# Kernel tuning notes

Hardware: AMD Instinct MI355X
Metric: run time of the kernel (lower is better)

## Reference

```python
import jax, jax.numpy as jnp
import numpy as np

B, T, INPUT_DIM, Z_DIM, RNN_DIM = 512, 200, 88, 100, 60


def setup_inputs() -> dict:
    key = jax.random.key(0)
    ks = jax.random.split(key, 18)
    sd = 0.05
    return {
        "mini_batch": jax.random.normal(ks[0], (B, T, INPUT_DIM), jnp.float32),
        "mini_batch_reversed": jax.random.normal(ks[1], (B, T, INPUT_DIM), jnp.float32),
        "mini_batch_mask": jnp.ones((B, T), jnp.float32),
        "mini_batch_seq_lengths": jax.random.randint(ks[2], (B,), T // 2, T + 1),
        "eps": jax.random.normal(ks[3], (T, B, Z_DIM), jnp.float32),
        # RNN (relu, 1 layer) params
        "W_ih": jax.random.normal(ks[4], (RNN_DIM, INPUT_DIM), jnp.float32) * sd,
        "W_hh": jax.random.normal(ks[5], (RNN_DIM, RNN_DIM), jnp.float32) * sd,
        "b_ih": jnp.zeros((RNN_DIM,), jnp.float32),
        "b_hh": jnp.zeros((RNN_DIM,), jnp.float32),
        "h_0": jax.random.normal(ks[6], (RNN_DIM,), jnp.float32),
        "z_q_0": jnp.zeros((Z_DIM,), jnp.float32),
        # Combiner params
        "W_zh": jax.random.normal(ks[7], (RNN_DIM, Z_DIM), jnp.float32) * sd,
        "b_zh": jnp.zeros((RNN_DIM,), jnp.float32),
        "W_hl": jax.random.normal(ks[8], (Z_DIM, RNN_DIM), jnp.float32) * sd,
        "b_hl": jnp.zeros((Z_DIM,), jnp.float32),
        "W_hs": jax.random.normal(ks[9], (Z_DIM, RNN_DIM), jnp.float32) * sd,
        "b_hs": jnp.zeros((Z_DIM,), jnp.float32),
    }


def _encoder(mini_batch_reversed, seq_lengths, eps,
             W_ih, W_hh, b_ih, b_hh, h_0, z_q_0,
             W_zh, b_zh, W_hl, b_hl, W_hs, b_hs):
    Bn = mini_batch_reversed.shape[0]
    Tn = mini_batch_reversed.shape[1]

    # --- relu RNN over reversed input, batch_first -> scan over time ---
    xs = jnp.transpose(mini_batch_reversed, (1, 0, 2))  # [T, B, input_dim]
    h0 = jnp.broadcast_to(h_0, (Bn, RNN_DIM))

    def rnn_step(h, x_t):
        h = jax.nn.relu(x_t @ W_ih.T + b_ih + h @ W_hh.T + b_hh)
        return h, h

    _, rnn_out = jax.lax.scan(rnn_step, h0, xs)          # [T, B, rnn_dim]
    rnn_out = jnp.transpose(rnn_out, (1, 0, 2))          # [B, T, rnn_dim]

    # --- pad_and_reverse: reverse each sequence by its length, zero-pad tail ---
    t_idx = jnp.arange(Tn)
    rev_idx = seq_lengths[:, None] - 1 - t_idx[None, :]  # [B, T]
    valid = rev_idx >= 0
    gathered = jnp.take_along_axis(rnn_out, jnp.clip(rev_idx, 0)[:, :, None], axis=1)
    rnn_rev = jnp.where(valid[:, :, None], gathered, 0.0)  # [B, T, rnn_dim]

    # --- sequential combiner + reparameterized sampling ---
    h_seq = jnp.transpose(rnn_rev, (1, 0, 2))            # [T, B, rnn_dim]
    z0 = jnp.broadcast_to(z_q_0, (Bn, Z_DIM))

    def comb_step(z_prev, inp):
        h_t, eps_t = inp
        h_comb = 0.5 * (jnp.tanh(z_prev @ W_zh.T + b_zh) + h_t)
        loc = h_comb @ W_hl.T + b_hl
        scale = jax.nn.softplus(h_comb @ W_hs.T + b_hs)
        z_t = loc + scale * eps_t
        return z_t, (z_t, loc, scale)

    _, (zs, locs, scales) = jax.lax.scan(comb_step, z0, (h_seq, eps))
    # [T, B, z] -> [B, T, z]
    tr = lambda a: jnp.transpose(a, (1, 0, 2))
    return tr(zs), tr(locs), tr(scales)


def reference(mini_batch, mini_batch_reversed, mini_batch_mask,
              mini_batch_seq_lengths, eps,
              W_ih, W_hh, b_ih, b_hh, h_0, z_q_0,
              W_zh, b_zh, W_hl, b_hl, W_hs, b_hs):
    return _encoder(mini_batch_reversed, mini_batch_seq_lengths, eps,
                    W_ih, W_hh, b_ih, b_hh, h_0, z_q_0,
                    W_zh, b_zh, W_hl, b_hl, W_hs, b_hs)
```

## Files before the change

### kernel.cpp

```cpp
#include <hip/hip_runtime.h>
#include <cmath>

#define NB 512
#define NT 200
#define NIN 88
#define NH 60
#define NZ 100

typedef float f2 __attribute__((ext_vector_type(2)));
typedef _Float16 h2v __attribute__((ext_vector_type(2)));
typedef _Float16 h8v __attribute__((ext_vector_type(8)));

__device__ __forceinline__ f2 pk_fma(f2 a, f2 b, f2 c) {
    return __builtin_elementwise_fma(a, b, c);
}
__device__ __forceinline__ float dot2(h2v a, h2v b, float c) {
#if __has_builtin(__builtin_amdgcn_fdot2)
    return __builtin_amdgcn_fdot2(a, b, c, false);
#else
    return fmaf((float)a.x, (float)b.x, fmaf((float)a.y, (float)b.y, c));
#endif
}
__device__ __forceinline__ float fast_tanh(float x) {
    float cx = fminf(fmaxf(x, -10.f), 10.f);
    float e  = __expf(2.f * cx);
    return (e - 1.f) * __builtin_amdgcn_rcpf(e + 1.f);
}
__device__ __forceinline__ float fast_softplus(float x) {
    return fmaxf(x, 0.f) + __logf(1.f + __expf(-fabsf(x)));
}
__device__ __forceinline__ void block_sync_lds() {
    asm volatile("s_waitcnt lgkmcnt(0)" ::: "memory");
    __builtin_amdgcn_s_barrier();
    asm volatile("" ::: "memory");
}

#define TCHUNKS 5
#define TCL (NT / TCHUNKS)

__global__ __launch_bounds__(128, 1)
void pre_kernel(const float* __restrict__ xrev, const float* __restrict__ W_ih,
                const float* __restrict__ b_ih, const float* __restrict__ b_hh,
                float* __restrict__ pre)
{
    __shared__ __align__(16) float xw[2][NIN];

    const int b    = blockIdx.x;
    const int tc   = blockIdx.y;
    const int wv   = threadIdx.x >> 6;
    const int lane = threadIdx.x & 63;

    f2 wih2[44];
    float bias = 0.f;
    if (lane < NH) {
        const float4* p = reinterpret_cast<const float4*>(W_ih + lane * NIN);
#pragma unroll
        for (int k = 0; k < 22; ++k) {
            float4 v = p[k];
            wih2[2*k]   = f2{v.x, v.y};
            wih2[2*k+1] = f2{v.z, v.w};
        }
        bias = b_ih[lane] + b_hh[lane];
    } else {
#pragma unroll
        for (int k = 0; k < 44; ++k) wih2[k] = f2{0.f, 0.f};
    }

    const float* xb = xrev + ((size_t)b * NT + (size_t)tc * TCL) * NIN;
    float* pb = pre + ((size_t)b * NT + (size_t)tc * TCL) * NH;

    float xa = xb[(size_t)wv * NIN + lane];
    float xc = (lane < NIN - 64) ? xb[(size_t)wv * NIN + 64 + lane] : 0.f;

    for (int k = 0; k < TCL / 2; ++k) {
        const int t = wv + 2 * k;
        xw[wv][lane] = xa;
        if (lane < NIN - 64) xw[wv][64 + lane] = xc;
        const int tn = t + 2;
        if (tn < TCL) {
            xa = xb[(size_t)tn * NIN + lane];
            xc = (lane < NIN - 64) ? xb[(size_t)tn * NIN + 64 + lane] : 0.f;
        }
        const float4* x4 = reinterpret_cast<const float4*>(xw[wv]);
        f2 a0 = f2{bias, 0.f}, a1 = f2{0.f, 0.f};
#pragma unroll
        for (int q = 0; q < 22; ++q) {
            float4 v = x4[q];
            a0 = pk_fma(f2{v.x, v.y}, wih2[2*q],   a0);
            a1 = pk_fma(f2{v.z, v.w}, wih2[2*q+1], a1);
        }
        if (lane < NH) pb[(size_t)t * NH + lane] = (a0.x + a1.x) + (a0.y + a1.y);
    }
}

__global__ __launch_bounds__(128, 1)
void fused1w(const int*   __restrict__ seqlen,
             const float* __restrict__ eps,
             const float* __restrict__ W_hh,
             const float* __restrict__ h0,
             const float* __restrict__ zq0,
             const float* __restrict__ W_zh,
             const float* __restrict__ b_zh,
             const float* __restrict__ W_hl,
             const float* __restrict__ b_hl,
             const float* __restrict__ W_hs,
             const float* __restrict__ b_hs,
             const float* __restrict__ pre,
             float* __restrict__ out)
{
    __shared__ __align__(16) _Float16 h_rev_h[2][NT][NH];
    __shared__ __align__(16) float    hbuf[2][64];
    __shared__ __align__(16) _Float16 zbh[2][112];
    __shared__ __align__(16) _Float16 hch[2][64];

    const int wv   = threadIdx.x >> 6;
    const int lane = threadIdx.x & 63;
    const int b    = blockIdx.x * 2 + wv;
    const int sl   = seqlen[b];

    {
        const int tail = (NT - sl) * NH;
        _Float16* base = &h_rev_h[wv][sl][0];
        for (int i = lane; i < tail; i += 64) base[i] = (_Float16)0;
    }
    if (lane < 12) zbh[wv][100 + lane] = (_Float16)0;
    if (lane >= NH) hch[wv][lane] = (_Float16)0;

    const bool oln = (lane < 50);
    const int  o1  = lane;
    const int  o2  = lane + 50;
    float e1 = 0.f, e2 = 0.f;
    if (oln) {
        zbh[wv][o1] = (_Float16)zq0[o1];
        zbh[wv][o2] = (_Float16)zq0[o2];
        e1 = eps[(size_t)b * NZ + o1];
        e2 = eps[(size_t)b * NZ + o2];
    }

    {
        f2 whh2[30];
        if (lane < NH) {
            const float4* q = reinterpret_cast<const float4*>(W_hh + lane * NH);
#pragma unroll
            for (int k = 0; k < 15; ++k) {
                float4 v = q[k];
                whh2[2*k]   = f2{v.x, v.y};
                whh2[2*k+1] = f2{v.z, v.w};
            }
            hbuf[wv][lane] = h0[lane];
        } else {
#pragma unroll
            for (int k = 0; k < 30; ++k) whh2[k] = f2{0.f, 0.f};
        }

        const float* pb = pre + (size_t)b * NT * NH;
        const bool hl = (lane < NH);
        float p0 = hl ? pb[0 * NH + lane] : 0.f;
        float p1 = hl ? pb[1 * NH + lane] : 0.f;
        float p2 = hl ? pb[2 * NH + lane] : 0.f;
        float p3 = hl ? pb[3 * NH + lane] : 0.f;
        for (int t = 0; t < NT; ++t) {
            float pn = (t + 4 < NT && hl) ? pb[(size_t)(t + 4) * NH + lane] : 0.f;
            const float4* h4 = reinterpret_cast<const float4*>(&hbuf[wv][0]);
            f2 a0 = f2{p0, 0.f}, a1 = f2{0.f, 0.f};
#pragma unroll
            for (int k = 0; k < 15; ++k) {
                float4 v = h4[k];
                a0 = pk_fma(f2{v.x, v.y}, whh2[2*k],   a0);
                a1 = pk_fma(f2{v.z, v.w}, whh2[2*k+1], a1);
            }
            float hn = fmaxf((a0.x + a1.x) + (a0.y + a1.y), 0.f);
            if (hl) {
                hbuf[wv][lane] = hn;
                if (t < sl) h_rev_h[wv][sl - 1 - t][lane] = (_Float16)hn;
            }
            p0 = p1; p1 = p2; p2 = p3; p3 = pn;
        }
    }

    h2v wzh_h[52];
    float bz = 0.f;
    if (lane < NH) {
        const float4* q = reinterpret_cast<const float4*>(W_zh + lane * NZ);
#pragma unroll
        for (int k = 0; k < 25; ++k) {
            float4 v = q[k];
            wzh_h[2*k]   = h2v{(_Float16)v.x, (_Float16)v.y};
            wzh_h[2*k+1] = h2v{(_Float16)v.z, (_Float16)v.w};
        }
        bz = b_zh[lane];
    } else {
#pragma unroll
        for (int k = 0; k < 50; ++k) wzh_h[k] = h2v{(_Float16)0, (_Float16)0};
    }
    wzh_h[50] = h2v{(_Float16)0, (_Float16)0};
    wzh_h[51] = wzh_h[50];

    h2v wlA[32], wsA[32], wlB[32], wsB[32];
    float blA = 0.f, bsA = 0.f, blB = 0.f, bsB = 0.f;
    if (oln) {
        const float4* pA = reinterpret_cast<const float4*>(W_hl + o1 * NH);
        const float4* qA = reinterpret_cast<const float4*>(W_hs + o1 * NH);
        const float4* pB = reinterpret_cast<const float4*>(W_hl + o2 * NH);
        const float4* qB = reinterpret_cast<const float4*>(W_hs + o2 * NH);
#pragma unroll
        for (int k = 0; k < 15; ++k) {
            float4 v;
            v = pA[k];
            wlA[2*k]   = h2v{(_Float16)(0.5f*v.x), (_Float16)(0.5f*v.y)};
            wlA[2*k+1] = h2v{(_Float16)(0.5f*v.z), (_Float16)(0.5f*v.w)};
            v = qA[k];
            wsA[2*k]   = h2v{(_Float16)(0.5f*v.x), (_Float16)(0.5f*v.y)};
            wsA[2*k+1] = h2v{(_Float16)(0.5f*v.z), (_Float16)(0.5f*v.w)};
            v = pB[k];
            wlB[2*k]   = h2v{(_Float16)(0.5f*v.x), (_Float16)(0.5f*v.y)};
            wlB[2*k+1] = h2v{(_Float16)(0.5f*v.z), (_Float16)(0.5f*v.w)};
            v = qB[k];
            wsB[2*k]   = h2v{(_Float16)(0.5f*v.x), (_Float16)(0.5f*v.y)};
            wsB[2*k+1] = h2v{(_Float16)(0.5f*v.z), (_Float16)(0.5f*v.w)};
        }
        blA = b_hl[o1]; bsA = b_hs[o1];
        blB = b_hl[o2]; bsB = b_hs[o2];
    } else {
#pragma unroll
        for (int k = 0; k < 32; ++k) {
            wlA[k] = h2v{(_Float16)0, (_Float16)0};
            wsA[k] = wlA[k]; wlB[k] = wlA[k]; wsB[k] = wlA[k];
        }
    }
    h2v zpad = h2v{(_Float16)0, (_Float16)0};
    wlA[30] = zpad; wlA[31] = zpad; wsA[30] = zpad; wsA[31] = zpad;
    wlB[30] = zpad; wlB[31] = zpad; wsB[30] = zpad; wsB[31] = zpad;

    float* out_z = out;
    float* out_l = out + (size_t)NB * NT * NZ;
    float* out_s = out + (size_t)2 * NB * NT * NZ;

    for (int t = 0; t < NT; ++t) {
        const h8v* z8 = reinterpret_cast<const h8v*>(&zbh[wv][0]);
        float za0 = 0.f, za1 = 0.f, za2 = 0.f, za3 = 0.f;
#pragma unroll
        for (int k = 0; k < 13; ++k) {
            h8v v = z8[k];
            za0 = dot2(h2v{v[0], v[1]}, wzh_h[4*k+0], za0);
            za1 = dot2(h2v{v[2], v[3]}, wzh_h[4*k+1], za1);
            za2 = dot2(h2v{v[4], v[5]}, wzh_h[4*k+2], za2);
            za3 = dot2(h2v{v[6], v[7]}, wzh_h[4*k+3], za3);
        }
        float hrow = (lane < NH) ? (float)h_rev_h[wv][t][lane] : 0.f;

        float e1n = 0.f, e2n = 0.f;
        if (oln && t + 1 < NT) {
            const float* ep = eps + ((size_t)(t + 1) * NB + b) * NZ;
            e1n = ep[o1];
            e2n = ep[o2];
        }

        if (lane < NH) {
            float a = (za0 + za1) + (za2 + za3) + bz;
            hch[wv][lane] = (_Float16)(fast_tanh(a) + hrow);
        }

        const h8v* h8p = reinterpret_cast<const h8v*>(&hch[wv][0]);
        float lA0 = 0.f, lA1 = 0.f, sA0 = 0.f, sA1 = 0.f;
        float lB0 = 0.f, lB1 = 0.f, sB0 = 0.f, sB1 = 0.f;
#pragma unroll
        for (int k = 0; k < 8; ++k) {
            h8v v = h8p[k];
            h2v x0 = h2v{v[0], v[1]}, x1 = h2v{v[2], v[3]};
            h2v x2 = h2v{v[4], v[5]}, x3 = h2v{v[6], v[7]};
            lA0 = dot2(x0, wlA[4*k+0], lA0);
            lA1 = dot2(x1, wlA[4*k+1], lA1);
            lA0 = dot2(x2, wlA[4*k+2], lA0);
            lA1 = dot2(x3, wlA[4*k+3], lA1);
            sA0 = dot2(x0, wsA[4*k+0], sA0);
            sA1 = dot2(x1, wsA[4*k+1], sA1);
            sA0 = dot2(x2, wsA[4*k+2], sA0);
            sA1 = dot2(x3, wsA[4*k+3], sA1);
            lB0 = dot2(x0, wlB[4*k+0], lB0);
            lB1 = dot2(x1, wlB[4*k+1], lB1);
            lB0 = dot2(x2, wlB[4*k+2], lB0);
            lB1 = dot2(x3, wlB[4*k+3], lB1);
            sB0 = dot2(x0, wsB[4*k+0], sB0);
            sB1 = dot2(x1, wsB[4*k+1], sB1);
            sB0 = dot2(x2, wsB[4*k+2], sB0);
            sB1 = dot2(x3, wsB[4*k+3], sB1);
        }
        if (oln) {
            float locA = lA0 + lA1 + blA;
            float psA  = sA0 + sA1 + bsA;
            float scA  = fast_softplus(psA);
            float zA   = locA + scA * e1;
            float locB = lB0 + lB1 + blB;
            float psB  = sB0 + sB1 + bsB;
            float scB  = fast_softplus(psB);
            float zB   = locB + scB * e2;
            size_t oi = ((size_t)b * NT + t) * NZ;
            out_z[oi + o1] = zA;  out_z[oi + o2] = zB;
            out_l[oi + o1] = locA; out_l[oi + o2] = locB;
            out_s[oi + o1] = scA;  out_s[oi + o2] = scB;
            zbh[wv][o1] = (_Float16)zA;
            zbh[wv][o2] = (_Float16)zB;
            e1 = e1n; e2 = e2n;
        }
    }
}

__global__ __launch_bounds__(128, 1)
void encoder_mono(const float* __restrict__ xrev, const int* __restrict__ seqlen,
                  const float* __restrict__ eps,
                  const float* __restrict__ W_ih, const float* __restrict__ W_hh,
                  const float* __restrict__ b_ih, const float* __restrict__ b_hh,
                  const float* __restrict__ h0,   const float* __restrict__ zq0,
                  const float* __restrict__ W_zh, const float* __restrict__ b_zh,
                  const float* __restrict__ W_hl, const float* __restrict__ b_hl,
                  const float* __restrict__ W_hs, const float* __restrict__ b_hs,
                  float* __restrict__ out)
{
    __shared__ __align__(16) float h_rev[NT][NH];
    __shared__ __align__(16) float xbuf[NIN];
    __shared__ __align__(16) float hbuf[NH];
    __shared__ __align__(16) float zbuf[NZ];
    __shared__ __align__(16) float hcomb[NH];

    const int b = blockIdx.x, tid = threadIdx.x;
    const int wave = tid >> 6, lane = tid & 63;
    const int sl = seqlen[b];

    for (int i = tid; i < NT * NH; i += 128) (&h_rev[0][0])[i] = 0.0f;
    __syncthreads();

    if (wave == 0) {
        float wih[NIN], whh[NH];
        float bias = 0.f;
        if (lane < NH) {
            const float4* pp = reinterpret_cast<const float4*>(W_ih + lane * NIN);
#pragma unroll
            for (int k = 0; k < NIN / 4; ++k) {
                float4 v = pp[k];
                wih[4*k+0]=v.x; wih[4*k+1]=v.y; wih[4*k+2]=v.z; wih[4*k+3]=v.w;
            }
            const float4* q = reinterpret_cast<const float4*>(W_hh + lane * NH);
#pragma unroll
            for (int k = 0; k < NH / 4; ++k) {
                float4 v = q[k];
                whh[4*k+0]=v.x; whh[4*k+1]=v.y; whh[4*k+2]=v.z; whh[4*k+3]=v.w;
            }
            bias = b_ih[lane] + b_hh[lane];
            hbuf[lane] = h0[lane];
        } else {
#pragma unroll
            for (int k = 0; k < NIN; ++k) wih[k] = 0.f;
#pragma unroll
            for (int k = 0; k < NH; ++k) whh[k] = 0.f;
        }
        const float* xb = xrev + (size_t)b * NT * NIN;
        float xa = xb[lane];
        float xc = (lane < NIN - 64) ? xb[64 + lane] : 0.f;
        for (int t = 0; t < NT; ++t) {
            xbuf[lane] = xa;
            if (lane < NIN - 64) xbuf[64 + lane] = xc;
            if (t + 1 < NT) {
                xa = xb[(size_t)(t+1)*NIN + lane];
                xc = (lane < NIN - 64) ? xb[(size_t)(t+1)*NIN + 64 + lane] : 0.f;
            }
            float a0=0.f,a1=0.f,a2=0.f,a3=0.f;
            const float4* x4 = reinterpret_cast<const float4*>(xbuf);
#pragma unroll
            for (int k = 0; k < NIN / 4; ++k) {
                float4 v = x4[k];
                a0 += v.x*wih[4*k+0]; a1 += v.y*wih[4*k+1];
                a2 += v.z*wih[4*k+2]; a3 += v.w*wih[4*k+3];
            }
            const float4* h4 = reinterpret_cast<const float4*>(hbuf);
#pragma unroll
            for (int k = 0; k < NH / 4; ++k) {
                float4 v = h4[k];
                a0 += v.x*whh[4*k+0]; a1 += v.y*whh[4*k+1];
                a2 += v.z*whh[4*k+2]; a3 += v.w*whh[4*k+3];
            }
            float hn = fmaxf((a0+a1)+(a2+a3)+bias, 0.f);
            if (lane < NH) {
                hbuf[lane] = hn;
                if (t < sl) h_rev[sl-1-t][lane] = hn;
            }
        }
    }
    __syncthreads();

    const int o = 50 * wave + lane;
    float wzr[NZ]; float bz = 0.f;
    if (wave == 0 && lane < NH) {
        const float4* pp = reinterpret_cast<const float4*>(W_zh + lane * NZ);
#pragma unroll
        for (int k = 0; k < NZ / 4; ++k) {
            float4 v = pp[k];
            wzr[4*k+0]=v.x; wzr[4*k+1]=v.y; wzr[4*k+2]=v.z; wzr[4*k+3]=v.w;
        }
        bz = b_zh[lane];
    } else {
#pragma unroll
        for (int k = 0; k < NZ; ++k) wzr[k] = 0.f;
    }
    float wl[NH], ws_[NH]; float bl = 0.f, bs = 0.f;
    if (lane < 50) {
        const float4* pp = reinterpret_cast<const float4*>(W_hl + o * NH);
        const float4* q  = reinterpret_cast<const float4*>(W_hs + o * NH);
#pragma unroll
        for (int k = 0; k < NH / 4; ++k) {
            float4 v = pp[k];
            wl[4*k+0]=v.x; wl[4*k+1]=v.y; wl[4*k+2]=v.z; wl[4*k+3]=v.w;
            float4 u = q[k];
            ws_[4*k+0]=u.x; ws_[4*k+1]=u.y; ws_[4*k+2]=u.z; ws_[4*k+3]=u.w;
        }
        bl = b_hl[o]; bs = b_hs[o];
        zbuf[o] = zq0[o];
    } else {
#pragma unroll
        for (int k = 0; k < NH; ++k) { wl[k]=0.f; ws_[k]=0.f; }
    }
    __syncthreads();

    float* out_z = out;
    float* out_l = out + (size_t)NB * NT * NZ;
    float* out_s = out + (size_t)2 * NB * NT * NZ;
    const float* epsb = eps + (size_t)b * NZ;
    float e_cur = (lane < 50) ? epsb[o] : 0.f;

    for (int t = 0; t < NT; ++t) {
        if (wave == 0) {
            float a0=0.f,a1=0.f,a2=0.f,a3=0.f;
            const float4* z4 = reinterpret_cast<const float4*>(zbuf);
#pragma unroll
            for (int k = 0; k < NZ / 4; ++k) {
                float4 v = z4[k];
                a0 += v.x*wzr[4*k+0]; a1 += v.y*wzr[4*k+1];
                a2 += v.z*wzr[4*k+2]; a3 += v.w*wzr[4*k+3];
            }
            if (lane < NH) {
                float a = (a0+a1)+(a2+a3)+bz;
                hcomb[lane] = 0.5f * (fast_tanh(a) + h_rev[t][lane]);
            }
        }
        block_sync_lds();
        float e_nxt = 0.f;
        if (t + 1 < NT && lane < 50) e_nxt = epsb[(size_t)(t+1)*NB*NZ + o];
        if (lane < 50) {
            float c0=0.f,c1=0.f,c2=0.f,c3=0.f, d0=0.f,d1=0.f,d2=0.f,d3=0.f;
            const float4* h4 = reinterpret_cast<const float4*>(hcomb);
#pragma unroll
            for (int k = 0; k < NH / 4; ++k) {
                float4 v = h4[k];
                c0 += v.x*wl[4*k+0];  c1 += v.y*wl[4*k+1];
                c2 += v.z*wl[4*k+2];  c3 += v.w*wl[4*k+3];
                d0 += v.x*ws_[4*k+0]; d1 += v.y*ws_[4*k+1];
                d2 += v.z*ws_[4*k+2]; d3 += v.w*ws_[4*k+3];
            }
            float loc = (c0+c1)+(c2+c3)+bl;
            float ps  = (d0+d1)+(d2+d3)+bs;
            float sc  = fast_softplus(ps);
            float zv  = loc + sc * e_cur;
            size_t oi = ((size_t)b * NT + t) * NZ + o;
            out_z[oi]=zv; out_l[oi]=loc; out_s[oi]=sc;
            zbuf[o]=zv;
        }
        e_cur = e_nxt;
        block_sync_lds();
    }
}

extern "C" void kernel_launch(void* const* d_in, const int* in_sizes, int n_in,
                              void* d_out, int out_size, void* d_ws, size_t ws_size,
                              hipStream_t stream) {
    const float* xrev   = (const float*)d_in[1];
    const int*   seqlen = (const int*)  d_in[3];
    const float* eps    = (const float*)d_in[4];
    const float* W_ih   = (const float*)d_in[5];
    const float* W_hh   = (const float*)d_in[6];
    const float* b_ih   = (const float*)d_in[7];
    const float* b_hh   = (const float*)d_in[8];
    const float* h0     = (const float*)d_in[9];
    const float* zq0    = (const float*)d_in[10];
    const float* W_zh   = (const float*)d_in[11];
    const float* b_zh   = (const float*)d_in[12];
    const float* W_hl   = (const float*)d_in[13];
    const float* b_hl   = (const float*)d_in[14];
    const float* W_hs   = (const float*)d_in[15];
    const float* b_hs   = (const float*)d_in[16];
    float* out = (float*)d_out;

    const size_t pre_bytes = (size_t)NB * NT * NH * sizeof(float);
    if (ws_size >= pre_bytes) {
        float* pre = (float*)d_ws;
        pre_kernel<<<dim3(NB, TCHUNKS), 128, 0, stream>>>(xrev, W_ih, b_ih, b_hh, pre);
        fused1w<<<NB / 2, 128, 0, stream>>>(seqlen, eps, W_hh, h0, zq0,
                                            W_zh, b_zh, W_hl, b_hl, W_hs, b_hs,
                                            pre, out);
    } else {
        encoder_mono<<<NB, 128, 0, stream>>>(xrev, seqlen, eps,
                                             W_ih, W_hh, b_ih, b_hh, h0, zq0,
                                             W_zh, b_zh, W_hl, b_hl, W_hs, b_hs,
                                             out);
    }
}
```

Baseline: 276.2 us.

## Process two batch elements per single wavefront with interleaved recurrences

The fused recurrent kernel now runs one 64-lane wavefront per block that advances two batch sequences together, interleaving their RNN and combiner dot products instead of assigning one wave per sequence. The aim is to hide per-step LDS and dependency latency through instruction-level parallelism and to share the register-resident weights. In exchange each wave does twice the serial work and uses more registers, and the two sequences no longer run on separate SIMDs in parallel.

```diff
diff --git a/kernel.cpp b/kernel.cpp
--- a/kernel.cpp
+++ b/kernel.cpp
@@ -93,8 +93,8 @@
     }
 }
 
-__global__ __launch_bounds__(128, 1)
-void fused1w(const int*   __restrict__ seqlen,
+__global__ __launch_bounds__(64, 1) __attribute__((amdgpu_waves_per_eu(1)))
+void fused2s(const int*   __restrict__ seqlen,
              const float* __restrict__ eps,
              const float* __restrict__ W_hh,
              const float* __restrict__ h0,
@@ -109,32 +109,41 @@
              float* __restrict__ out)
 {
     __shared__ __align__(16) _Float16 h_rev_h[2][NT][NH];
-    __shared__ __align__(16) float    hbuf[2][64];
+    __shared__ __align__(16) float    hbufF[2][64];
     __shared__ __align__(16) _Float16 zbh[2][112];
     __shared__ __align__(16) _Float16 hch[2][64];
 
-    const int wv   = threadIdx.x >> 6;
-    const int lane = threadIdx.x & 63;
-    const int b    = blockIdx.x * 2 + wv;
-    const int sl   = seqlen[b];
+    const int lane = threadIdx.x;
+    const int b0   = blockIdx.x * 2;
+    const int b1   = b0 + 1;
+    const int sl0  = seqlen[b0];
+    const int sl1  = seqlen[b1];
 
     {
-        const int tail = (NT - sl) * NH;
-        _Float16* base = &h_rev_h[wv][sl][0];
-        for (int i = lane; i < tail; i += 64) base[i] = (_Float16)0;
-    }
-    if (lane < 12) zbh[wv][100 + lane] = (_Float16)0;
-    if (lane >= NH) hch[wv][lane] = (_Float16)0;
+        const int tail = (NT - sl0) * NH;
+        _Float16* p = &h_rev_h[0][sl0][0];
+        for (int i = lane; i < tail; i += 64) p[i] = (_Float16)0;
+    }
+    {
+        const int tail = (NT - sl1) * NH;
+        _Float16* p = &h_rev_h[1][sl1][0];
+        for (int i = lane; i < tail; i += 64) p[i] = (_Float16)0;
+    }
+    if (lane < 12) { zbh[0][100 + lane] = (_Float16)0; zbh[1][100 + lane] = (_Float16)0; }
+    if (lane >= NH) { hch[0][lane] = (_Float16)0; hch[1][lane] = (_Float16)0; }
 
     const bool oln = (lane < 50);
     const int  o1  = lane;
     const int  o2  = lane + 50;
-    float e1 = 0.f, e2 = 0.f;
+    float e1_0 = 0.f, e2_0 = 0.f, e1_1 = 0.f, e2_1 = 0.f;
     if (oln) {
-        zbh[wv][o1] = (_Float16)zq0[o1];
-        zbh[wv][o2] = (_Float16)zq0[o2];
-        e1 = eps[(size_t)b * NZ + o1];
-        e2 = eps[(size_t)b * NZ + o2];
+        float zA = zq0[o1], zB = zq0[o2];
+        zbh[0][o1] = (_Float16)zA; zbh[0][o2] = (_Float16)zB;
+        zbh[1][o1] = (_Float16)zA; zbh[1][o2] = (_Float16)zB;
+        e1_0 = eps[(size_t)b0 * NZ + o1];
+        e2_0 = eps[(size_t)b0 * NZ + o2];
+        e1_1 = eps[(size_t)b1 * NZ + o1];
+        e2_1 = eps[(size_t)b1 * NZ + o2];
     }
 
     {
@@ -147,34 +156,48 @@
                 whh2[2*k]   = f2{v.x, v.y};
                 whh2[2*k+1] = f2{v.z, v.w};
             }
-            hbuf[wv][lane] = h0[lane];
+            float hv = h0[lane];
+            hbufF[0][lane] = hv;
+            hbufF[1][lane] = hv;
         } else {
 #pragma unroll
             for (int k = 0; k < 30; ++k) whh2[k] = f2{0.f, 0.f};
         }
 
-        const float* pb = pre + (size_t)b * NT * NH;
+        const float* pbA = pre + (size_t)b0 * NT * NH;
+        const float* pbB = pre + (size_t)b1 * NT * NH;
         const bool hl = (lane < NH);
-        float p0 = hl ? pb[0 * NH + lane] : 0.f;
-        float p1 = hl ? pb[1 * NH + lane] : 0.f;
-        float p2 = hl ? pb[2 * NH + lane] : 0.f;
-        float p3 = hl ? pb[3 * NH + lane] : 0.f;
+        float p0a = hl ? pbA[0*NH + lane] : 0.f, p0b = hl ? pbB[0*NH + lane] : 0.f;
+        float p1a = hl ? pbA[1*NH + lane] : 0.f, p1b = hl ? pbB[1*NH + lane] : 0.f;
+        float p2a = hl ? pbA[2*NH + lane] : 0.f, p2b = hl ? pbB[2*NH + lane] : 0.f;
+        float p3a = hl ? pbA[3*NH + lane] : 0.f, p3b = hl ? pbB[3*NH + lane] : 0.f;
+
         for (int t = 0; t < NT; ++t) {
-            float pn = (t + 4 < NT && hl) ? pb[(size_t)(t + 4) * NH + lane] : 0.f;
-            const float4* h4 = reinterpret_cast<const float4*>(&hbuf[wv][0]);
-            f2 a0 = f2{p0, 0.f}, a1 = f2{0.f, 0.f};
+            float pna = (t + 4 < NT && hl) ? pbA[(size_t)(t + 4) * NH + lane] : 0.f;
+            float pnb = (t + 4 < NT && hl) ? pbB[(size_t)(t + 4) * NH + lane] : 0.f;
+            const float4* h4a = reinterpret_cast<const float4*>(&hbufF[0][0]);
+            const float4* h4b = reinterpret_cast<const float4*>(&hbufF[1][0]);
+            f2 a0 = f2{p0a, 0.f}, a1 = f2{0.f, 0.f};
+            f2 c0 = f2{p0b, 0.f}, c1 = f2{0.f, 0.f};
 #pragma unroll
             for (int k = 0; k < 15; ++k) {
-                float4 v = h4[k];
-                a0 = pk_fma(f2{v.x, v.y}, whh2[2*k],   a0);
-                a1 = pk_fma(f2{v.z, v.w}, whh2[2*k+1], a1);
-            }
-            float hn = fmaxf((a0.x + a1.x) + (a0.y + a1.y), 0.f);
+                float4 va = h4a[k];
+                a0 = pk_fma(f2{va.x, va.y}, whh2[2*k],   a0);
+                a1 = pk_fma(f2{va.z, va.w}, whh2[2*k+1], a1);
+                float4 vb = h4b[k];
+                c0 = pk_fma(f2{vb.x, vb.y}, whh2[2*k],   c0);
+                c1 = pk_fma(f2{vb.z, vb.w}, whh2[2*k+1], c1);
+            }
+            float hnA = fmaxf((a0.x + a1.x) + (a0.y + a1.y), 0.f);
+            float hnB = fmaxf((c0.x + c1.x) + (c0.y + c1.y), 0.f);
             if (hl) {
-                hbuf[wv][lane] = hn;
-                if (t < sl) h_rev_h[wv][sl - 1 - t][lane] = (_Float16)hn;
-            }
-            p0 = p1; p1 = p2; p2 = p3; p3 = pn;
+                hbufF[0][lane] = hnA;
+                hbufF[1][lane] = hnB;
+                if (t < sl0) h_rev_h[0][sl0 - 1 - t][lane] = (_Float16)hnA;
+                if (t < sl1) h_rev_h[1][sl1 - 1 - t][lane] = (_Float16)hnB;
+            }
+            p0a = p1a; p1a = p2a; p2a = p3a; p3a = pna;
+            p0b = p1b; p1b = p2b; p2b = p3b; p3b = pnb;
         }
     }
 
@@ -228,80 +251,134 @@
             wsA[k] = wlA[k]; wlB[k] = wlA[k]; wsB[k] = wlA[k];
         }
     }
-    h2v zpad = h2v{(_Float16)0, (_Float16)0};
-    wlA[30] = zpad; wlA[31] = zpad; wsA[30] = zpad; wsA[31] = zpad;
-    wlB[30] = zpad; wlB[31] = zpad; wsB[30] = zpad; wsB[31] = zpad;
+    {
+        h2v zp = h2v{(_Float16)0, (_Float16)0};
+        wlA[30] = zp; wlA[31] = zp; wsA[30] = zp; wsA[31] = zp;
+        wlB[30] = zp; wlB[31] = zp; wsB[30] = zp; wsB[31] = zp;
+    }
 
     float* out_z = out;
     float* out_l = out + (size_t)NB * NT * NZ;
     float* out_s = out + (size_t)2 * NB * NT * NZ;
 
     for (int t = 0; t < NT; ++t) {
-        const h8v* z8 = reinterpret_cast<const h8v*>(&zbh[wv][0]);
-        float za0 = 0.f, za1 = 0.f, za2 = 0.f, za3 = 0.f;
+        const h8v* z80 = reinterpret_cast<const h8v*>(&zbh[0][0]);
+        const h8v* z81 = reinterpret_cast<const h8v*>(&zbh[1][0]);
+        float za0_0 = 0.f, za1_0 = 0.f, za2_0 = 0.f, za3_0 = 0.f;
+        float za0_1 = 0.f, za1_1 = 0.f, za2_1 = 0.f, za3_1 = 0.f;
 #pragma unroll
         for (int k = 0; k < 13; ++k) {
-            h8v v = z8[k];
-            za0 = dot2(h2v{v[0], v[1]}, wzh_h[4*k+0], za0);
-            za1 = dot2(h2v{v[2], v[3]}, wzh_h[4*k+1], za1);
-            za2 = dot2(h2v{v[4], v[5]}, wzh_h[4*k+2], za2);
-            za3 = dot2(h2v{v[6], v[7]}, wzh_h[4*k+3], za3);
-        }
-        float hrow = (lane < NH) ? (float)h_rev_h[wv][t][lane] : 0.f;
-
-        float e1n = 0.f, e2n = 0.f;
+            h8v v0 = z80[k];
+            za0_0 = dot2(h2v{v0[0], v0[1]}, wzh_h[4*k+0], za0_0);
+            za1_0 = dot2(h2v{v0[2], v0[3]}, wzh_h[4*k+1], za1_0);
+            za2_0 = dot2(h2v{v0[4], v0[5]}, wzh_h[4*k+2], za2_0);
+            za3_0 = dot2(h2v{v0[6], v0[7]}, wzh_h[4*k+3], za3_0);
+            h8v v1 = z81[k];
+            za0_1 = dot2(h2v{v1[0], v1[1]}, wzh_h[4*k+0], za0_1);
+            za1_1 = dot2(h2v{v1[2], v1[3]}, wzh_h[4*k+1], za1_1);
+            za2_1 = dot2(h2v{v1[4], v1[5]}, wzh_h[4*k+2], za2_1);
+            za3_1 = dot2(h2v{v1[6], v1[7]}, wzh_h[4*k+3], za3_1);
+        }
+        float hrow0 = (lane < NH) ? (float)h_rev_h[0][t][lane] : 0.f;
+        float hrow1 = (lane < NH) ? (float)h_rev_h[1][t][lane] : 0.f;
+
+        float e1n_0 = 0.f, e2n_0 = 0.f, e1n_1 = 0.f, e2n_1 = 0.f;
         if (oln && t + 1 < NT) {
-            const float* ep = eps + ((size_t)(t + 1) * NB + b) * NZ;
-            e1n = ep[o1];
-            e2n = ep[o2];
+            const float* ep0 = eps + ((size_t)(t + 1) * NB + b0) * NZ;
+            const float* ep1 = eps + ((size_t)(t + 1) * NB + b1) * NZ;
+            e1n_0 = ep0[o1]; e2n_0 = ep0[o2];
+            e1n_1 = ep1[o1]; e2n_1 = ep1[o2];
         }
 
         if (lane < NH) {
-            float a = (za0 + za1) + (za2 + za3) + bz;
-            hch[wv][lane] = (_Float16)(fast_tanh(a) + hrow);
-        }
-
-        const h8v* h8p = reinterpret_cast<const h8v*>(&hch[wv][0]);
-        float lA0 = 0.f, lA1 = 0.f, sA0 = 0.f, sA1 = 0.f;
-        float lB0 = 0.f, lB1 = 0.f, sB0 = 0.f, sB1 = 0.f;
+            float a0 = (za0_0 + za1_0) + (za2_0 + za3_0) + bz;
+            float a1 = (za0_1 + za1_1) + (za2_1 + za3_1) + bz;
+            hch[0][lane] = (_Float16)(fast_tanh(a0) + hrow0);
+            hch[1][lane] = (_Float16)(fast_tanh(a1) + hrow1);
+        }
+
+        const h8v* hp0 = reinterpret_cast<const h8v*>(&hch[0][0]);
+        const h8v* hp1 = reinterpret_cast<const h8v*>(&hch[1][0]);
+        float lA_0 = 0.f, lAx_0 = 0.f, sA_0 = 0.f, sAx_0 = 0.f;
+        float lB_0 = 0.f, lBx_0 = 0.f, sB_0 = 0.f, sBx_0 = 0.f;
+        float lA_1 = 0.f, lAx_1 = 0.f, sA_1 = 0.f, sAx_1 = 0.f;
+        float lB_1 = 0.f, lBx_1 = 0.f, sB_1 = 0.f, sBx_1 = 0.f;
 #pragma unroll
         for (int k = 0; k < 8; ++k) {
-            h8v v = h8p[k];
-            h2v x0 = h2v{v[0], v[1]}, x1 = h2v{v[2], v[3]};
-            h2v x2 = h2v{v[4], v[5]}, x3 = h2v{v[6], v[7]};
-            lA0 = dot2(x0, wlA[4*k+0], lA0);
-            lA1 = dot2(x1, wlA[4*k+1], lA1);
-            lA0 = dot2(x2, wlA[4*k+2], lA0);
-            lA1 = dot2(x3, wlA[4*k+3], lA1);
-            sA0 = dot2(x0, wsA[4*k+0], sA0);
-            sA1 = dot2(x1, wsA[4*k+1], sA1);
-            sA0 = dot2(x2, wsA[4*k+2], sA0);
-            sA1 = dot2(x3, wsA[4*k+3], sA1);
-            lB0 = dot2(x0, wlB[4*k+0], lB0);
-            lB1 = dot2(x1, wlB[4*k+1], lB1);
-            lB0 = dot2(x2, wlB[4*k+2], lB0);
-            lB1 = dot2(x3, wlB[4*k+3], lB1);
-            sB0 = dot2(x0, wsB[4*k+0], sB0);
-            sB1 = dot2(x1, wsB[4*k+1], sB1);
-            sB0 = dot2(x2, wsB[4*k+2], sB0);
-            sB1 = dot2(x3, wsB[4*k+3], sB1);
+            h8v v0 = hp0[k];
+            h2v x00 = h2v{v0[0], v0[1]}, x01 = h2v{v0[2], v0[3]};
+            h2v x02 = h2v{v0[4], v0[5]}, x03 = h2v{v0[6], v0[7]};
+            lA_0  = dot2(x00, wlA[4*k+0], lA_0);
+            lAx_0 = dot2(x01, wlA[4*k+1], lAx_0);
+            lA_0  = dot2(x02, wlA[4*k+2], lA_0);
+            lAx_0 = dot2(x03, wlA[4*k+3], lAx_0);
+            sA_0  = dot2(x00, wsA[4*k+0], sA_0);
+            sAx_0 = dot2(x01, wsA[4*k+1], sAx_0);
+            sA_0  = dot2(x02, wsA[4*k+2], sA_0);
+            sAx_0 = dot2(x03, wsA[4*k+3], sAx_0);
+            lB_0  = dot2(x00, wlB[4*k+0], lB_0);
+            lBx_0 = dot2(x01, wlB[4*k+1], lBx_0);
+            lB_0  = dot2(x02, wlB[4*k+2], lB_0);
+            lBx_0 = dot2(x03, wlB[4*k+3], lBx_0);
+            sB_0  = dot2(x00, wsB[4*k+0], sB_0);
+            sBx_0 = dot2(x01, wsB[4*k+1], sBx_0);
+            sB_0  = dot2(x02, wsB[4*k+2], sB_0);
+            sBx_0 = dot2(x03, wsB[4*k+3], sBx_0);
+            h8v v1 = hp1[k];
+            h2v x10 = h2v{v1[0], v1[1]}, x11 = h2v{v1[2], v1[3]};
+            h2v x12 = h2v{v1[4], v1[5]}, x13 = h2v{v1[6], v1[7]};
+            lA_1  = dot2(x10, wlA[4*k+0], lA_1);
+            lAx_1 = dot2(x11, wlA[4*k+1], lAx_1);
+            lA_1  = dot2(x12, wlA[4*k+2], lA_1);
+            lAx_1 = dot2(x13, wlA[4*k+3], lAx_1);
+            sA_1  = dot2(x10, wsA[4*k+0], sA_1);
+            sAx_1 = dot2(x11, wsA[4*k+1], sAx_1);
+            sA_1  = dot2(x12, wsA[4*k+2], sA_1);
+            sAx_1 = dot2(x13, wsA[4*k+3], sAx_1);
+            lB_1  = dot2(x10, wlB[4*k+0], lB_1);
+            lBx_1 = dot2(x11, wlB[4*k+1], lBx_1);
+            lB_1  = dot2(x12, wlB[4*k+2], lB_1);
+            lBx_1 = dot2(x13, wlB[4*k+3], lBx_1);
+            sB_1  = dot2(x10, wsB[4*k+0], sB_1);
+            sBx_1 = dot2(x11, wsB[4*k+1], sBx_1);
+            sB_1  = dot2(x12, wsB[4*k+2], sB_1);
+            sBx_1 = dot2(x13, wsB[4*k+3], sBx_1);
         }
         if (oln) {
-            float locA = lA0 + lA1 + blA;
-            float psA  = sA0 + sA1 + bsA;
-            float scA  = fast_softplus(psA);
-            float zA   = locA + scA * e1;
-            float locB = lB0 + lB1 + blB;
-            float psB  = sB0 + sB1 + bsB;
-            float scB  = fast_softplus(psB);
-            float zB   = locB + scB * e2;
-            size_t oi = ((size_t)b * NT + t) * NZ;
-            out_z[oi + o1] = zA;  out_z[oi + o2] = zB;
-            out_l[oi + o1] = locA; out_l[oi + o2] = locB;
-            out_s[oi + o1] = scA;  out_s[oi + o2] = scB;
-            zbh[wv][o1] = (_Float16)zA;
-            zbh[wv][o2] = (_Float16)zB;
-            e1 = e1n; e2 = e2n;
+            {
+                float locA = lA_0 + lAx_0 + blA;
+                float psA  = sA_0 + sAx_0 + bsA;
+                float scA  = fast_softplus(psA);
+                float zA   = locA + scA * e1_0;
+                float locB = lB_0 + lBx_0 + blB;
+                float psB  = sB_0 + sBx_0 + bsB;
+                float scB  = fast_softplus(psB);
+                float zB   = locB + scB * e2_0;
+                size_t oi = ((size_t)b0 * NT + t) * NZ;
+                out_z[oi + o1] = zA;   out_z[oi + o2] = zB;
+                out_l[oi + o1] = locA; out_l[oi + o2] = locB;
+                out_s[oi + o1] = scA;  out_s[oi + o2] = scB;
+                zbh[0][o1] = (_Float16)zA;
+                zbh[0][o2] = (_Float16)zB;
+                e1_0 = e1n_0; e2_0 = e2n_0;
+            }
+            {
+                float locA = lA_1 + lAx_1 + blA;
+                float psA  = sA_1 + sAx_1 + bsA;
+                float scA  = fast_softplus(psA);
+                float zA   = locA + scA * e1_1;
+                float locB = lB_1 + lBx_1 + blB;
+                float psB  = sB_1 + sBx_1 + bsB;
+                float scB  = fast_softplus(psB);
+                float zB   = locB + scB * e2_1;
+                size_t oi = ((size_t)b1 * NT + t) * NZ;
+                out_z[oi + o1] = zA;   out_z[oi + o2] = zB;
+                out_l[oi + o1] = locA; out_l[oi + o2] = locB;
+                out_s[oi + o1] = scA;  out_s[oi + o2] = scB;
+                zbh[1][o1] = (_Float16)zA;
+                zbh[1][o2] = (_Float16)zB;
+                e1_1 = e1n_1; e2_1 = e2n_1;
+            }
         }
     }
 }
@@ -493,9 +570,9 @@
     if (ws_size >= pre_bytes) {
         float* pre = (float*)d_ws;
         pre_kernel<<<dim3(NB, TCHUNKS), 128, 0, stream>>>(xrev, W_ih, b_ih, b_hh, pre);
-        fused1w<<<NB / 2, 128, 0, stream>>>(seqlen, eps, W_hh, h0, zq0,
-                                            W_zh, b_zh, W_hl, b_hl, W_hs, b_hs,
-                                            pre, out);
+        fused2s<<<NB / 2, 64, 0, stream>>>(seqlen, eps, W_hh, h0, zq0,
+                                           W_zh, b_zh, W_hl, b_hl, W_hs, b_hs,
+                                           pre, out);
     } else {
         encoder_mono<<<NB, 128, 0, stream>>>(xrev, seqlen, eps,
                                              W_ih, W_hh, b_ih, b_hh, h0, zq0,
```

New measurement: 474.7 us. 71.9% more time.

## Move combiner output weights from registers to shared LDS with software prefetch

Applied to the files above, without the earlier changes.

The fp16 W_hl/W_hs weight registers (128 h2v per lane) are replaced by a shared LDS table that both waves fill cooperatively, since each wave's lanes need the same output rows. Inside the per-step loop the weights are streamed from LDS with a one-chunk-ahead prefetch. The goal is to relieve register pressure or spilling in the recurrent kernel. In exchange, every timestep now issues about 32 extra 16-byte LDS reads per lane that sit on the sequential critical path.

```diff
diff --git a/kernel.cpp b/kernel.cpp
--- a/kernel.cpp
+++ b/kernel.cpp
@@ -20,6 +20,12 @@
 #else
     return fmaf((float)a.x, (float)b.x, fmaf((float)a.y, (float)b.y, c));
 #endif
+}
+__device__ __forceinline__ void dot8(h8v x, h8v w, float& p, float& q) {
+    p = dot2(h2v{x[0], x[1]}, h2v{w[0], w[1]}, p);
+    q = dot2(h2v{x[2], x[3]}, h2v{w[2], w[3]}, q);
+    p = dot2(h2v{x[4], x[5]}, h2v{w[4], w[5]}, p);
+    q = dot2(h2v{x[6], x[7]}, h2v{w[6], w[7]}, q);
 }
 __device__ __forceinline__ float fast_tanh(float x) {
     float cx = fminf(fmaxf(x, -10.f), 10.f);
@@ -92,6 +98,8 @@
         if (lane < NH) pb[(size_t)t * NH + lane] = (a0.x + a1.x) + (a0.y + a1.y);
     }
 }
+
+#define WOUT_BYTES (8 * 64 * 80)
 
 __global__ __launch_bounds__(128, 1)
 void fused1w(const int*   __restrict__ seqlen,
@@ -112,6 +120,7 @@
     __shared__ __align__(16) float    hbuf[2][64];
     __shared__ __align__(16) _Float16 zbh[2][112];
     __shared__ __align__(16) _Float16 hch[2][64];
+    __shared__ __align__(16) char     wout[WOUT_BYTES];
 
     const int wv   = threadIdx.x >> 6;
     const int lane = threadIdx.x & 63;
@@ -135,6 +144,41 @@
         zbh[wv][o2] = (_Float16)zq0[o2];
         e1 = eps[(size_t)b * NZ + o1];
         e2 = eps[(size_t)b * NZ + o2];
+    }
+
+    {
+        const int r0 = 2 * wv, r1 = 2 * wv + 1;
+        if (oln) {
+            const int  oo   = (wv == 0) ? o1 : o2;
+            const float* s0 = W_hl + oo * NH;
+            const float* s1 = W_hs + oo * NH;
+#pragma unroll
+            for (int r = 0; r < 2; ++r) {
+                const float* src = (r == 0) ? s0 : s1;
+                const int rr = (r == 0) ? r0 : r1;
+                float tmp[64];
+#pragma unroll
+                for (int j = 0; j < NH; ++j) tmp[j] = 0.5f * src[j];
+#pragma unroll
+                for (int j = NH; j < 64; ++j) tmp[j] = 0.f;
+#pragma unroll
+                for (int k = 0; k < 8; ++k) {
+                    h8v h;
+#pragma unroll
+                    for (int e = 0; e < 8; ++e) h[e] = (_Float16)tmp[8*k+e];
+                    *reinterpret_cast<h8v*>(wout + k*5120 + lane*80 + rr*16) = h;
+                }
+            }
+        } else {
+            h8v zz;
+#pragma unroll
+            for (int e = 0; e < 8; ++e) zz[e] = (_Float16)0;
+#pragma unroll
+            for (int k = 0; k < 8; ++k) {
+                *reinterpret_cast<h8v*>(wout + k*5120 + lane*80 + r0*16) = zz;
+                *reinterpret_cast<h8v*>(wout + k*5120 + lane*80 + r1*16) = zz;
+            }
+        }
     }
 
     {
@@ -196,45 +240,24 @@
     wzh_h[50] = h2v{(_Float16)0, (_Float16)0};
     wzh_h[51] = wzh_h[50];
 
-    h2v wlA[32], wsA[32], wlB[32], wsB[32];
     float blA = 0.f, bsA = 0.f, blB = 0.f, bsB = 0.f;
     if (oln) {
-        const float4* pA = reinterpret_cast<const float4*>(W_hl + o1 * NH);
-        const float4* qA = reinterpret_cast<const float4*>(W_hs + o1 * NH);
-        const float4* pB = reinterpret_cast<const float4*>(W_hl + o2 * NH);
-        const float4* qB = reinterpret_cast<const float4*>(W_hs + o2 * NH);
-#pragma unroll
-        for (int k = 0; k < 15; ++k) {
-            float4 v;
-            v = pA[k];
-            wlA[2*k]   = h2v{(_Float16)(0.5f*v.x), (_Float16)(0.5f*v.y)};
-            wlA[2*k+1] = h2v{(_Float16)(0.5f*v.z), (_Float16)(0.5f*v.w)};
-            v = qA[k];
-            wsA[2*k]   = h2v{(_Float16)(0.5f*v.x), (_Float16)(0.5f*v.y)};
-            wsA[2*k+1] = h2v{(_Float16)(0.5f*v.z), (_Float16)(0.5f*v.w)};
-            v = pB[k];
-            wlB[2*k]   = h2v{(_Float16)(0.5f*v.x), (_Float16)(0.5f*v.y)};
-            wlB[2*k+1] = h2v{(_Float16)(0.5f*v.z), (_Float16)(0.5f*v.w)};
-            v = qB[k];
-            wsB[2*k]   = h2v{(_Float16)(0.5f*v.x), (_Float16)(0.5f*v.y)};
-            wsB[2*k+1] = h2v{(_Float16)(0.5f*v.z), (_Float16)(0.5f*v.w)};
-        }
         blA = b_hl[o1]; bsA = b_hs[o1];
         blB = b_hl[o2]; bsB = b_hs[o2];
-    } else {
-#pragma unroll
-        for (int k = 0; k < 32; ++k) {
-            wlA[k] = h2v{(_Float16)0, (_Float16)0};
-            wsA[k] = wlA[k]; wlB[k] = wlA[k]; wsB[k] = wlA[k];
-        }
-    }
-    h2v zpad = h2v{(_Float16)0, (_Float16)0};
-    wlA[30] = zpad; wlA[31] = zpad; wsA[30] = zpad; wsA[31] = zpad;
-    wlB[30] = zpad; wlB[31] = zpad; wsB[30] = zpad; wsB[31] = zpad;
+    }
+
+    block_sync_lds();
 
     float* out_z = out;
     float* out_l = out + (size_t)NB * NT * NZ;
     float* out_s = out + (size_t)2 * NB * NT * NZ;
+
+    const char* wbase = wout + lane * 80;
+
+    h8v pf0 = *reinterpret_cast<const h8v*>(wbase + 0*5120 + 0);
+    h8v pf1 = *reinterpret_cast<const h8v*>(wbase + 0*5120 + 16);
+    h8v pf2 = *reinterpret_cast<const h8v*>(wbase + 0*5120 + 32);
+    h8v pf3 = *reinterpret_cast<const h8v*>(wbase + 0*5120 + 48);
 
     for (int t = 0; t < NT; ++t) {
         const h8v* z8 = reinterpret_cast<const h8v*>(&zbh[wv][0]);
@@ -262,29 +285,25 @@
         }
 
         const h8v* h8p = reinterpret_cast<const h8v*>(&hch[wv][0]);
+        h8v c0 = pf0, c1 = pf1, c2 = pf2, c3 = pf3;
         float lA0 = 0.f, lA1 = 0.f, sA0 = 0.f, sA1 = 0.f;
         float lB0 = 0.f, lB1 = 0.f, sB0 = 0.f, sB1 = 0.f;
 #pragma unroll
         for (int k = 0; k < 8; ++k) {
-            h8v v = h8p[k];
-            h2v x0 = h2v{v[0], v[1]}, x1 = h2v{v[2], v[3]};
-            h2v x2 = h2v{v[4], v[5]}, x3 = h2v{v[6], v[7]};
-            lA0 = dot2(x0, wlA[4*k+0], lA0);
-            lA1 = dot2(x1, wlA[4*k+1], lA1);
-            lA0 = dot2(x2, wlA[4*k+2], lA0);
-            lA1 = dot2(x3, wlA[4*k+3], lA1);
-            sA0 = dot2(x0, wsA[4*k+0], sA0);
-            sA1 = dot2(x1, wsA[4*k+1], sA1);
-            sA0 = dot2(x2, wsA[4*k+2], sA0);
-            sA1 = dot2(x3, wsA[4*k+3], sA1);
-            lB0 = dot2(x0, wlB[4*k+0], lB0);
-            lB1 = dot2(x1, wlB[4*k+1], lB1);
-            lB0 = dot2(x2, wlB[4*k+2], lB0);
-            lB1 = dot2(x3, wlB[4*k+3], lB1);
-            sB0 = dot2(x0, wsB[4*k+0], sB0);
-            sB1 = dot2(x1, wsB[4*k+1], sB1);
-            sB0 = dot2(x2, wsB[4*k+2], sB0);
-            sB1 = dot2(x3, wsB[4*k+3], sB1);
+            h8v n0, n1, n2, n3;
+            if (k < 7) {
+                const char* nb = wbase + (k + 1) * 5120;
+                n0 = *reinterpret_cast<const h8v*>(nb + 0);
+                n1 = *reinterpret_cast<const h8v*>(nb + 16);
+                n2 = *reinterpret_cast<const h8v*>(nb + 32);
+                n3 = *reinterpret_cast<const h8v*>(nb + 48);
+            }
+            h8v x = h8p[k];
+            dot8(x, c0, lA0, lA1);
+            dot8(x, c1, sA0, sA1);
+            dot8(x, c2, lB0, lB1);
+            dot8(x, c3, sB0, sB1);
+            if (k < 7) { c0 = n0; c1 = n1; c2 = n2; c3 = n3; }
         }
         if (oln) {
             float locA = lA0 + lA1 + blA;
@@ -296,12 +315,18 @@
             float scB  = fast_softplus(psB);
             float zB   = locB + scB * e2;
             size_t oi = ((size_t)b * NT + t) * NZ;
-            out_z[oi + o1] = zA;  out_z[oi + o2] = zB;
+            out_z[oi + o1] = zA;   out_z[oi + o2] = zB;
             out_l[oi + o1] = locA; out_l[oi + o2] = locB;
             out_s[oi + o1] = scA;  out_s[oi + o2] = scB;
             zbh[wv][o1] = (_Float16)zA;
             zbh[wv][o2] = (_Float16)zB;
             e1 = e1n; e2 = e2n;
+        }
+        if (t + 1 < NT) {
+            pf0 = *reinterpret_cast<const h8v*>(wbase + 0*5120 + 0);
+            pf1 = *reinterpret_cast<const h8v*>(wbase + 0*5120 + 16);
+            pf2 = *reinterpret_cast<const h8v*>(wbase + 0*5120 + 32);
+            pf3 = *reinterpret_cast<const h8v*>(wbase + 0*5120 + 48);
         }
     }
 }
```

Result: faster. 254.6 us (-7.8%).
